# Optimization experiments

Hardware: AMD Instinct MI355X
Metric: run time of the kernel (lower is better)

Reference implementation:

```python
import jax, jax.numpy as jnp
import numpy as np

K = 16          # neighbors per point
POINTNUM = 2048 # opt.pointnum
B, N = 8, 2048


def _knn_concat(x, k):
    """x: [B,N,C] -> [B,N,k,2C] = concat(center, k-nearest neighbor feats)."""
    sq = jnp.sum(x * x, axis=-1)                                   # [B,N]
    d2 = sq[:, :, None] + sq[:, None, :] - 2.0 * jnp.einsum('bnc,bmc->bnm', x, x)
    _, idx = jax.lax.top_k(-d2, k)                                 # [B,N,k]
    nbr = jax.vmap(lambda xb, ib: xb[ib])(x, idx)                  # [B,N,k,C]
    ctr = jnp.broadcast_to(x[:, :, None, :], nbr.shape)
    return jnp.concatenate([ctr, nbr], axis=-1)


def _lin(x, w, b):
    return x @ w + b


lrelu = jax.nn.leaky_relu  # default negative_slope=0.01 matches nn.LeakyReLU()


def setup_inputs() -> dict:
    key = jax.random.key(0)
    ks = jax.random.split(key, 20)

    def w(k_, fi, fo):
        return jax.random.normal(k_, (fi, fo), jnp.float32) / np.sqrt(fi)

    inp = {
        'x': jax.random.normal(ks[0], (B, N, 3), jnp.float32),
        'h1w1': w(ks[1], 6, 16),   'h1b1': jnp.zeros((16,), jnp.float32),
        'h1w2': w(ks[2], 16, 64),  'h1b2': jnp.zeros((64,), jnp.float32),
        'h1w3': w(ks[3], 64, 32),  'h1b3': jnp.zeros((32,), jnp.float32),
        'h2w1': w(ks[4], 64, 256), 'h2b1': jnp.zeros((256,), jnp.float32),
        'h2w2': w(ks[5], 256, 128),'h2b2': jnp.zeros((128,), jnp.float32),
        'h3w1': w(ks[6], 256, 128),'h3b1': jnp.zeros((128,), jnp.float32),
        'fc1w': w(ks[7], 128, 128),'fc1b': jnp.zeros((128,), jnp.float32),
        'fc2w': w(ks[8], 128, 128),'fc2b': jnp.zeros((128,), jnp.float32),
        'fc3w': w(ks[9], 128, POINTNUM * 3), 'fc3b': jnp.zeros((POINTNUM * 3,), jnp.float32),
    }
    return inp


def reference(x, h1w1, h1b1, h1w2, h1b2, h1w3, h1b3,
              h2w1, h2b1, h2w2, h2b2, h3w1, h3b1,
              fc1w, fc1b, fc2w, fc2b, fc3w, fc3b):
    # block 1: knn-concat [B,N,K,6] -> MLP(6,16,64,32) -> sum over K
    x1 = _knn_concat(x, K)
    h = lrelu(_lin(x1, h1w1, h1b1))
    h = lrelu(_lin(h, h1w2, h1b2))
    h = lrelu(_lin(h, h1w3, h1b3))
    x2 = jnp.sum(h, axis=2)                    # [B,N,32]
    # block 2: [B,N,K,64] -> MLP(64,256,128) -> sum over K
    x2 = _knn_concat(x2, K)
    h = lrelu(_lin(x2, h2w1, h2b1))
    h = lrelu(_lin(h, h2w2, h2b2))
    x3 = jnp.sum(h, axis=2)                    # [B,N,128]
    # block 3: [B,N,K,256] -> MLP(256,128) -> sum over K
    x3 = _knn_concat(x3, K)
    h = lrelu(_lin(x3, h3w1, h3b1))
    x4 = jnp.sum(h, axis=2)                    # [B,N,128]
    # global max pool over points
    x5 = jnp.max(x4, axis=1)                   # [B,128]
    x6 = lrelu(_lin(x5, fc1w, fc1b))
    x7 = lrelu(_lin(x6, fc2w, fc2b))
    x8 = _lin(x7, fc3w, fc3b)                  # [B, POINTNUM*3]
    return x8.reshape(x8.shape[0], POINTNUM, 3)
```

## Files before the change

kernel.cpp:

```cpp
#include <hip/hip_runtime.h>

#define KNB 16
#define BSZ 8
#define NPT 2048

typedef __attribute__((ext_vector_type(8))) short bf16x8;
typedef __attribute__((ext_vector_type(4))) float f32x4;

__device__ __forceinline__ float lrelu(float x) { return x >= 0.f ? x : 0.01f * x; }

__device__ __forceinline__ unsigned short bf16rne(float f) {
    union { float f; unsigned int u; } v; v.f = f;
    return (unsigned short)((v.u + 0x7FFFu + ((v.u >> 16) & 1u)) >> 16);
}

__device__ __forceinline__ float packkey(float d, int idx) {
    union { float f; unsigned int u; } v; v.f = d;
    v.u = (v.u & 0xFFFFF800u) | (unsigned int)idx;
    return v.f;
}

__device__ __forceinline__ void ceA(float& a, float& b) {
    const float lo = fminf(a, b), hi = fmaxf(a, b);
    a = lo; b = hi;
}

__device__ __forceinline__ void bsort16(float* c) {
#pragma unroll
    for (int k = 2; k <= 16; k <<= 1) {
#pragma unroll
        for (int j = k >> 1; j > 0; j >>= 1) {
#pragma unroll
            for (int i = 0; i < 16; ++i) {
                const int l = i ^ j;
                if (l > i) {
                    if ((i & k) == 0) ceA(c[i], c[l]);
                    else              ceA(c[l], c[i]);
                }
            }
        }
    }
}

__device__ __forceinline__ void merge16(float* L, const float* C) {
#pragma unroll
    for (int i = 0; i < 16; ++i) L[i] = fminf(L[i], C[15 - i]);
#pragma unroll
    for (int j = 8; j > 0; j >>= 1) {
#pragma unroll
        for (int i = 0; i < 16; ++i) {
            const int l = i ^ j;
            if (l > i) ceA(L[i], L[l]);
        }
    }
}

__device__ __forceinline__ void st16(float* dst, const float* L) {
#pragma unroll
    for (int c = 0; c < 4; ++c)
        *(f32x4*)(dst + c * 4) = (f32x4){L[c * 4], L[c * 4 + 1], L[c * 4 + 2], L[c * 4 + 3]};
}

__device__ __forceinline__ void ld16(float* L, const float* src) {
#pragma unroll
    for (int c = 0; c < 4; ++c) {
        const f32x4 v = *(const f32x4*)(src + c * 4);
        L[c * 4] = v[0]; L[c * 4 + 1] = v[1]; L[c * 4 + 2] = v[2]; L[c * 4 + 3] = v[3];
    }
}

__device__ __forceinline__ void xwave_merge_out(float (*sS)[20], int w, int lane,
                                                float* L, float* outp) {
    st16(sS[w * 64 + lane], L);
    __syncthreads();
    if ((w & 1) == 0) {
        float C[16];
        ld16(C, sS[(w + 1) * 64 + lane]);
        merge16(L, C);
        if (w == 2) st16(sS[2 * 64 + lane], L);
    }
    __syncthreads();
    if (w == 0) {
        float C[16];
        ld16(C, sS[2 * 64 + lane]);
        merge16(L, C);
        st16(outp, L);
    }
}

__global__ void wprep_kernel(const float* __restrict__ w, unsigned short* __restrict__ wt,
                             int K, int N) {
    int i = blockIdx.x * 256 + threadIdx.x;
    if (i < K * N) { int k = i / N, n = i - k * N; wt[n * K + k] = bf16rne(w[i]); }
}

__global__ void wprep_b1_kernel(const float* __restrict__ w1, const float* __restrict__ w2,
                                const float* __restrict__ w3,
                                unsigned short* __restrict__ w1a, unsigned short* __restrict__ w2a,
                                unsigned short* __restrict__ w3a) {
    int i = blockIdx.x * 256 + threadIdx.x;
    if (i < 512) {
        int n = i >> 5, k = i & 31;
        w1a[i] = (k < 6) ? bf16rne(w1[k * 16 + n]) : (unsigned short)0;
    } else if (i < 2560) {
        int j = i - 512, n = j >> 5, k = j & 31;
        w2a[j] = (k < 16) ? bf16rne(w2[k * 64 + n]) : (unsigned short)0;
    } else if (i < 4608) {
        int j = i - 2560, n = j >> 6, k = j & 63;
        w3a[j] = bf16rne(w3[k * 32 + n]);
    }
}

template<int C>
__global__ void norms16_kernel(const unsigned short* __restrict__ feat, float* __restrict__ out) {
    int gid = blockIdx.x * blockDim.x + threadIdx.x;
    if (gid < BSZ * NPT) {
        const unsigned short* p = feat + (size_t)gid * C;
        float s = 0.f;
#pragma unroll
        for (int c8 = 0; c8 < C / 8; ++c8) {
            const bf16x8 v = *(const bf16x8*)(p + c8 * 8);
#pragma unroll
            for (int j = 0; j < 8; ++j) {
                union { unsigned int u; float f; } t;
                t.u = ((unsigned int)(unsigned short)v[j]) << 16;
                s = fmaf(t.f, t.f, s);
            }
        }
        out[gid] = s;
    }
}

template<int C>
__global__ void norms_kernel(const float* __restrict__ feat, float* __restrict__ out) {
    int gid = blockIdx.x * blockDim.x + threadIdx.x;
    if (gid < BSZ * NPT) {
        const float* p = feat + (size_t)gid * C;
        float s = 0.f;
#pragma unroll
        for (int c = 0; c < C; ++c) s = fmaf(p[c], p[c], s);
        out[gid] = s;
    }
}

template<int JS>
__launch_bounds__(256, 3)
__global__ void knn3_kernel(const float* __restrict__ feat,
                            const float* __restrict__ norms,
                            float* __restrict__ cand) {
    constexpr int JL = NPT / JS;
    constexpr int JP = JL / 4;
    const int b = blockIdx.z, js = blockIdx.y, i0 = blockIdx.x * 64;
    const int t = threadIdx.x, w = t >> 6, lane = t & 63;
    const float* fb = feat + (size_t)b * NPT * 3;
    const float* nb = norms + (size_t)b * NPT;

    __shared__ __align__(16) float sS[256][20];

    float q0, q1, q2;
    { const float* qp = fb + (size_t)(i0 + lane) * 3; q0 = qp[0]; q1 = qp[1]; q2 = qp[2]; }

    float L[16];
#pragma unroll
    for (int u = 0; u < 16; ++u) L[u] = 3e38f;

    const int jbeg = js * JL + w * JP;
#pragma unroll 1
    for (int j0 = jbeg; j0 < jbeg + JP; j0 += 16) {
        float C[16];
#pragma unroll
        for (int u = 0; u < 16; ++u) {
            const int j = j0 + u;
            const float* pp = fb + (size_t)j * 3;
            C[u] = packkey(fmaf(-2.f, fmaf(q0, pp[0], fmaf(q1, pp[1], q2 * pp[2])), nb[j]), j);
        }
        bsort16(C);
        merge16(L, C);
    }
    float* o = cand + (((size_t)b * NPT + i0 + lane) * JS + js) * 16;
    xwave_merge_out(sS, w, lane, L, o);
}

template<int C, int JS>
__launch_bounds__(256, 3)
__global__ void knn_mfma_kernel(const unsigned short* __restrict__ fb16,
                                const float* __restrict__ norms,
                                float* __restrict__ cand) {
    constexpr int JL = NPT / JS;
    constexpr int KS = C / 32;
    const int b    = blockIdx.z;
    const int js   = blockIdx.y;
    const int i0   = blockIdx.x * 64;
    const int t    = threadIdx.x;
    const int w    = t >> 6;
    const int lane = t & 63;
    const int l15  = lane & 15;
    const int quad = lane >> 4;
    const unsigned short* fbb = fb16 + (size_t)b * NPT * C;
    const float* nb = norms + (size_t)b * NPT;

    __shared__ __align__(16) float sS[256][20];

    bf16x8 afr[KS * 4];
#pragma unroll
    for (int ks = 0; ks < KS; ++ks)
#pragma unroll
        for (int mi = 0; mi < 4; ++mi)
            afr[ks * 4 + mi] = *(const bf16x8*)(fbb + (size_t)(i0 + mi * 16 + l15) * C + ks * 32 + quad * 8);

    float L[16];
#pragma unroll
    for (int u = 0; u < 16; ++u) L[u] = 3e38f;

    const int jbeg = js * JL;
#pragma unroll 1
    for (int j0 = jbeg; j0 < jbeg + JL; j0 += 64) {
        f32x4 acc[4];
#pragma unroll
        for (int mi = 0; mi < 4; ++mi) acc[mi] = (f32x4){0.f, 0.f, 0.f, 0.f};
        const unsigned short* prow = fbb + (size_t)(j0 + w * 16 + l15) * C + quad * 8;
#pragma unroll
        for (int ks = 0; ks < KS; ++ks) {
            const bf16x8 bfr = *(const bf16x8*)(prow + ks * 32);
#pragma unroll
            for (int mi = 0; mi < 4; ++mi)
                acc[mi] = __builtin_amdgcn_mfma_f32_16x16x32_bf16(afr[ks * 4 + mi], bfr, acc[mi], 0, 0, 0);
        }
        const float nv  = nb[j0 + w * 16 + l15];
        const int  cidx = j0 + w * 16 + l15;
#pragma unroll
        for (int mi = 0; mi < 4; ++mi)
#pragma unroll
            for (int r = 0; r < 4; ++r)
                sS[w * 64 + mi * 16 + quad * 4 + r][l15] = packkey(fmaf(-2.f, acc[mi][r], nv), cidx);
        float Cb[16];
        ld16(Cb, sS[w * 64 + lane]);
        bsort16(Cb);
        merge16(L, Cb);
    }

    float* o = cand + (((size_t)b * NPT + i0 + lane) * JS + js) * 16;
    xwave_merge_out(sS, w, lane, L, o);
}

template<int JS>
__launch_bounds__(256)
__global__ void knn_merge_kernel(const float* __restrict__ cand, int* __restrict__ knn_out) {
    const int q = blockIdx.x * 256 + threadIdx.x;
    const float* pd = cand + (size_t)q * JS * 16;
    float L[16];
    ld16(L, pd);
#pragma unroll
    for (int s = 1; s < JS; ++s) {
        float C[16];
        ld16(C, pd + s * 16);
        merge16(L, C);
    }
    int* o = knn_out + (size_t)q * KNB;
#pragma unroll
    for (int u = 0; u < 16; ++u) {
        union { float f; unsigned int v; } z; z.f = L[u];
        o[u] = (int)(z.v & 2047u);
    }
}

__launch_bounds__(256, 3)
__global__ void block1_mfma_kernel(const float* __restrict__ x, const int* __restrict__ knn,
                                   const unsigned short* __restrict__ w1a, const float* __restrict__ b1,
                                   const unsigned short* __restrict__ w2a, const float* __restrict__ b2,
                                   const unsigned short* __restrict__ w3a, const float* __restrict__ b3,
                                   unsigned short* __restrict__ x2b) {
    const int w = threadIdx.x >> 6, lane = threadIdx.x & 63;
    const int l15 = lane & 15, quad = lane >> 4;

    const bf16x8 W1 = *(const bf16x8*)(w1a + l15 * 32 + quad * 8);
    bf16x8 W2[4];
#pragma unroll
    for (int nt = 0; nt < 4; ++nt)
        W2[nt] = *(const bf16x8*)(w2a + (nt * 16 + l15) * 32 + quad * 8);
    bf16x8 W3[2][2];
#pragma unroll
    for (int tt = 0; tt < 2; ++tt)
#pragma unroll
        for (int ks = 0; ks < 2; ++ks)
            W3[tt][ks] = *(const bf16x8*)(w3a + (tt * 16 + l15) * 64 + ks * 32 + quad * 8);
    float b1v[4], b2v[4][4], b3v[2][4];
#pragma unroll
    for (int r = 0; r < 4; ++r) b1v[r] = b1[quad * 4 + r];
#pragma unroll
    for (int nt = 0; nt < 4; ++nt)
#pragma unroll
        for (int r = 0; r < 4; ++r) b2v[nt][r] = b2[nt * 16 + quad * 4 + r];
#pragma unroll
    for (int tt = 0; tt < 2; ++tt)
#pragma unroll
        for (int r = 0; r < 4; ++r) b3v[tt][r] = b3[tt * 16 + quad * 4 + r];

    const int src0 = ((2 * quad) & 3) * 16 + l15;
    const int src1 = ((2 * quad + 1) & 3) * 16 + l15;
    const int ntsel = quad >> 1;

    const int p0 = blockIdx.x * 16 + w * 4;
#pragma unroll 2
    for (int pi = 0; pi < 4; ++pi) {
        const int p = p0 + pi, b = p >> 11, n = p & (NPT - 1);
        int d0 = 0, d1 = 0, d2 = 0;
        if (quad == 0) {
            const float* xc = x + ((size_t)b * NPT + n) * 3;
            const int jn = knn[(size_t)p * KNB + l15];
            const float* xn = x + ((size_t)b * NPT + jn) * 3;
            const unsigned s0 = bf16rne(xc[0]), s1 = bf16rne(xc[1]), s2 = bf16rne(xc[2]);
            const unsigned s3 = bf16rne(xn[0]), s4 = bf16rne(xn[1]), s5 = bf16rne(xn[2]);
            d0 = (int)(s0 | (s1 << 16));
            d1 = (int)(s2 | (s3 << 16));
            d2 = (int)(s4 | (s5 << 16));
        }
        union { int i[4]; bf16x8 v; } B1;
        B1.i[0] = d0; B1.i[1] = d1; B1.i[2] = d2; B1.i[3] = 0;
        const f32x4 a1 = __builtin_amdgcn_mfma_f32_16x16x32_bf16(W1, B1.v, (f32x4){0.f, 0.f, 0.f, 0.f}, 0, 0, 0);

        int h10, h11;
        {
            const unsigned t0 = bf16rne(lrelu(a1[0] + b1v[0]));
            const unsigned t1 = bf16rne(lrelu(a1[1] + b1v[1]));
            const unsigned t2 = bf16rne(lrelu(a1[2] + b1v[2]));
            const unsigned t3 = bf16rne(lrelu(a1[3] + b1v[3]));
            h10 = (int)(t0 | (t1 << 16));
            h11 = (int)(t2 | (t3 << 16));
        }
        union { int i[4]; bf16x8 v; } B2;
        {
            const int e0 = __shfl(h10, src0), e1 = __shfl(h11, src0);
            const int e2 = __shfl(h10, src1), e3 = __shfl(h11, src1);
            const bool val = quad < 2;
            B2.i[0] = val ? e0 : 0; B2.i[1] = val ? e1 : 0;
            B2.i[2] = val ? e2 : 0; B2.i[3] = val ? e3 : 0;
        }
        f32x4 a2[4];
#pragma unroll
        for (int nt = 0; nt < 4; ++nt)
            a2[nt] = __builtin_amdgcn_mfma_f32_16x16x32_bf16(W2[nt], B2.v, (f32x4){0.f, 0.f, 0.f, 0.f}, 0, 0, 0);
        int dpk[4][2];
#pragma unroll
        for (int nt = 0; nt < 4; ++nt) {
            const unsigned t0 = bf16rne(lrelu(a2[nt][0] + b2v[nt][0]));
            const unsigned t1 = bf16rne(lrelu(a2[nt][1] + b2v[nt][1]));
            const unsigned t2 = bf16rne(lrelu(a2[nt][2] + b2v[nt][2]));
            const unsigned t3 = bf16rne(lrelu(a2[nt][3] + b2v[nt][3]));
            dpk[nt][0] = (int)(t0 | (t1 << 16));
            dpk[nt][1] = (int)(t2 | (t3 << 16));
        }
        f32x4 a3[2] = { (f32x4){0.f, 0.f, 0.f, 0.f}, (f32x4){0.f, 0.f, 0.f, 0.f} };
#pragma unroll
        for (int ks = 0; ks < 2; ++ks) {
            union { int i[4]; bf16x8 v; } B3;
            const int a0l = __shfl(dpk[2 * ks][0], src0), a0h = __shfl(dpk[2 * ks + 1][0], src0);
            const int a1l = __shfl(dpk[2 * ks][1], src0), a1h = __shfl(dpk[2 * ks + 1][1], src0);
            const int a2l = __shfl(dpk[2 * ks][0], src1), a2h = __shfl(dpk[2 * ks + 1][0], src1);
            const int a3l = __shfl(dpk[2 * ks][1], src1), a3h = __shfl(dpk[2 * ks + 1][1], src1);
            B3.i[0] = ntsel ? a0h : a0l;
            B3.i[1] = ntsel ? a1h : a1l;
            B3.i[2] = ntsel ? a2h : a2l;
            B3.i[3] = ntsel ? a3h : a3l;
#pragma unroll
            for (int tt = 0; tt < 2; ++tt)
                a3[tt] = __builtin_amdgcn_mfma_f32_16x16x32_bf16(W3[tt][ks], B3.v, a3[tt], 0, 0, 0);
        }
#pragma unroll
        for (int tt = 0; tt < 2; ++tt) {
#pragma unroll
            for (int r = 0; r < 4; ++r) {
                float s = lrelu(a3[tt][r] + b3v[tt][r]);
                s += __shfl_xor(s, 1);
                s += __shfl_xor(s, 2);
                s += __shfl_xor(s, 4);
                s += __shfl_xor(s, 8);
                if (l15 == 0)
                    x2b[(size_t)p * 32 + tt * 16 + quad * 4 + r] = bf16rne(s);
            }
        }
    }
}

__launch_bounds__(256, 2)
__global__ void block2_fused_kernel(const unsigned short* __restrict__ x2b,
                                    const int* __restrict__ knn,
                                    const unsigned short* __restrict__ w1t,
                                    const float* __restrict__ b1,
                                    const unsigned short* __restrict__ w2t,
                                    const float* __restrict__ b2,
                                    unsigned short* __restrict__ x3b) {
    const int w    = threadIdx.x >> 6;
    const int lane = threadIdx.x & 63;
    const int l15  = lane & 15, quad = lane >> 4;
    __shared__ __align__(16) unsigned short sH1[2][16][264];

    bf16x8 B1[4][2];
#pragma unroll
    for (int nt2 = 0; nt2 < 4; ++nt2)
#pragma unroll
        for (int ks = 0; ks < 2; ++ks)
            B1[nt2][ks] = *(const bf16x8*)(w1t + (size_t)(w * 64 + nt2 * 16 + l15) * 64 + ks * 32 + quad * 8);
    bf16x8 B2[2][8];
#pragma unroll
    for (int nt2 = 0; nt2 < 2; ++nt2)
#pragma unroll
        for (int ks = 0; ks < 8; ++ks)
            B2[nt2][ks] = *(const bf16x8*)(w2t + (size_t)(w * 32 + nt2 * 16 + l15) * 256 + ks * 32 + quad * 8);
    float b1v[4];
#pragma unroll
    for (int nt2 = 0; nt2 < 4; ++nt2) b1v[nt2] = b1[w * 64 + nt2 * 16 + l15];
    float b2v[2];
#pragma unroll
    for (int nt2 = 0; nt2 < 2; ++nt2) b2v[nt2] = b2[w * 32 + nt2 * 16 + l15];

    const int p0 = blockIdx.x * 8;
    const unsigned short* xb = x2b + (size_t)(p0 >> 11) * NPT * 32;

    int nbrv[8];
#pragma unroll
    for (int pi = 0; pi < 8; ++pi) nbrv[pi] = knn[(size_t)(p0 + pi) * KNB + l15];

    auto L1 = [&](const bf16x8& a0, const bf16x8& a1, int wbuf) {
#pragma unroll
        for (int nt2 = 0; nt2 < 4; ++nt2) {
            f32x4 acc = (f32x4){0.f, 0.f, 0.f, 0.f};
            acc = __builtin_amdgcn_mfma_f32_16x16x32_bf16(a0, B1[nt2][0], acc, 0, 0, 0);
            acc = __builtin_amdgcn_mfma_f32_16x16x32_bf16(a1, B1[nt2][1], acc, 0, 0, 0);
#pragma unroll
            for (int r = 0; r < 4; ++r)
                sH1[wbuf][quad * 4 + r][w * 64 + nt2 * 16 + l15] = bf16rne(lrelu(acc[r] + b1v[nt2]));
        }
    };
    auto L2 = [&](int p, int buf) {
        bf16x8 af[8];
#pragma unroll
        for (int ks = 0; ks < 8; ++ks)
            af[ks] = *(const bf16x8*)&sH1[buf][l15][ks * 32 + quad * 8];
#pragma unroll
        for (int nt2 = 0; nt2 < 2; ++nt2) {
            f32x4 acc = (f32x4){0.f, 0.f, 0.f, 0.f};
#pragma unroll
            for (int ks = 0; ks < 8; ++ks)
                acc = __builtin_amdgcn_mfma_f32_16x16x32_bf16(af[ks], B2[nt2][ks], acc, 0, 0, 0);
            float s = 0.f;
#pragma unroll
            for (int r = 0; r < 4; ++r) s += lrelu(acc[r] + b2v[nt2]);
            s += __shfl_xor(s, 16);
            s += __shfl_xor(s, 32);
            if (quad == 0) x3b[(size_t)p * 128 + w * 32 + nt2 * 16 + l15] = bf16rne(s);
        }
    };

    bf16x8 a0A = *(const bf16x8*)(x2b + (size_t)p0 * 32 + quad * 8);
    bf16x8 a1A = *(const bf16x8*)(xb + (size_t)nbrv[0] * 32 + quad * 8);
    bf16x8 a0B = *(const bf16x8*)(x2b + (size_t)(p0 + 1) * 32 + quad * 8);
    bf16x8 a1B = *(const bf16x8*)(xb + (size_t)nbrv[1] * 32 + quad * 8);
    L1(a0A, a1A, 0);

#pragma unroll
    for (int pj = 0; pj < 4; ++pj) {
        __syncthreads();
        L2(p0 + 2 * pj, 0);
        if (pj < 3) {
            a0A = *(const bf16x8*)(x2b + (size_t)(p0 + 2 * pj + 2) * 32 + quad * 8);
            a1A = *(const bf16x8*)(xb + (size_t)nbrv[2 * pj + 2] * 32 + quad * 8);
        }
        L1(a0B, a1B, 1);
        __syncthreads();
        L2(p0 + 2 * pj + 1, 1);
        if (pj < 3) {
            a0B = *(const bf16x8*)(x2b + (size_t)(p0 + 2 * pj + 3) * 32 + quad * 8);
            a1B = *(const bf16x8*)(xb + (size_t)nbrv[2 * pj + 3] * 32 + quad * 8);
            L1(a0A, a1A, 0);
        }
    }
}

__launch_bounds__(256, 3)
__global__ void block3_fused_kernel(const unsigned short* __restrict__ x3b,
                                    const int* __restrict__ knn,
                                    const unsigned short* __restrict__ w3t,
                                    const float* __restrict__ bias,
                                    float* __restrict__ x4) {
    const int w    = threadIdx.x >> 6;
    const int lane = threadIdx.x & 63;
    const int l15  = lane & 15, quad = lane >> 4;

    bf16x8 B3[2][8];
#pragma unroll
    for (int nt2 = 0; nt2 < 2; ++nt2)
#pragma unroll
        for (int ks = 0; ks < 8; ++ks)
            B3[nt2][ks] = *(const bf16x8*)(w3t + (size_t)(w * 32 + nt2 * 16 + l15) * 256 + ks * 32 + quad * 8);
    float bv[2];
#pragma unroll
    for (int nt2 = 0; nt2 < 2; ++nt2) bv[nt2] = bias[w * 32 + nt2 * 16 + l15];

    const int p0 = blockIdx.x * 8;
    const unsigned short* xb = x3b + (size_t)(p0 >> 11) * NPT * 128;

    int nbrv[8];
#pragma unroll
    for (int pi = 0; pi < 8; ++pi) nbrv[pi] = knn[(size_t)(p0 + pi) * KNB + l15];

    auto LDAF = [&](bf16x8* af, int pi, int nbr) {
        const unsigned short* ctr = x3b + (size_t)(p0 + pi) * 128 + quad * 8;
        const unsigned short* nbp = xb + (size_t)nbr * 128 + quad * 8;
#pragma unroll
        for (int ks = 0; ks < 4; ++ks) af[ks] = *(const bf16x8*)(ctr + ks * 32);
#pragma unroll
        for (int ks = 0; ks < 4; ++ks) af[4 + ks] = *(const bf16x8*)(nbp + ks * 32);
    };
    auto CMP = [&](int p, const bf16x8* af) {
#pragma unroll
        for (int nt2 = 0; nt2 < 2; ++nt2) {
            f32x4 acc = (f32x4){0.f, 0.f, 0.f, 0.f};
#pragma unroll
            for (int ks = 0; ks < 8; ++ks)
                acc = __builtin_amdgcn_mfma_f32_16x16x32_bf16(af[ks], B3[nt2][ks], acc, 0, 0, 0);
            float s = 0.f;
#pragma unroll
            for (int r = 0; r < 4; ++r) s += lrelu(acc[r] + bv[nt2]);
            s += __shfl_xor(s, 16);
            s += __shfl_xor(s, 32);
            if (quad == 0) x4[(size_t)p * 128 + w * 32 + nt2 * 16 + l15] = s;
        }
    };

    bf16x8 afA[8], afB[8];
    LDAF(afA, 0, nbrv[0]);
#pragma unroll
    for (int pj = 0; pj < 4; ++pj) {
        LDAF(afB, 2 * pj + 1, nbrv[2 * pj + 1]);
        CMP(p0 + 2 * pj, afA);
        if (pj < 3) LDAF(afA, 2 * pj + 2, nbrv[2 * pj + 2]);
        CMP(p0 + 2 * pj + 1, afB);
    }
}

__launch_bounds__(128)
__global__ void maxpool_partial_kernel(const float* __restrict__ x4,
                                       float* __restrict__ part) {
    const int chunk = blockIdx.x, b = blockIdx.y, t = threadIdx.x;
    const float* xb = x4 + ((size_t)b * NPT + (size_t)chunk * 128) * 128;
    float m = -1e30f;
#pragma unroll 8
    for (int n = 0; n < 128; ++n) m = fmaxf(m, xb[(size_t)n * 128 + t]);
    part[((size_t)b * 16 + chunk) * 128 + t] = m;
}

__launch_bounds__(128)
__global__ void head2_kernel(const float* __restrict__ part,
                             const float* __restrict__ fc1w, const float* __restrict__ fc1b,
                             const float* __restrict__ fc2w, const float* __restrict__ fc2b,
                             const float* __restrict__ fc3w, const float* __restrict__ fc3b,
                             float* __restrict__ out) {
    const int g = blockIdx.x, b = blockIdx.y, t = threadIdx.x;
    __shared__ float s5[128], s6[128], s7[128];
    float m = -1e30f;
#pragma unroll
    for (int c = 0; c < 16; ++c)
        m = fmaxf(m, part[((size_t)b * 16 + c) * 128 + t]);
    s5[t] = m;
    __syncthreads();
    float a = fc1b[t];
#pragma unroll 4
    for (int i = 0; i < 128; ++i) a = fmaf(s5[i], fc1w[i * 128 + t], a);
    s6[t] = lrelu(a);
    __syncthreads();
    a = fc2b[t];
#pragma unroll 4
    for (int i = 0; i < 128; ++i) a = fmaf(s6[i], fc2w[i * 128 + t], a);
    s7[t] = lrelu(a);
    __syncthreads();
    const int o = g * 128 + t;
    float acc = fc3b[o];
#pragma unroll 4
    for (int i = 0; i < 128; ++i) acc = fmaf(s7[i], fc3w[(size_t)i * 6144 + o], acc);
    out[(size_t)b * 6144 + o] = acc;
}

extern "C" void kernel_launch(void* const* d_in, const int* in_sizes, int n_in,
                              void* d_out, int out_size, void* d_ws, size_t ws_size,
                              hipStream_t stream) {
    const float* x    = (const float*)d_in[0];
    const float* h1w1 = (const float*)d_in[1];
    const float* h1b1 = (const float*)d_in[2];
    const float* h1w2 = (const float*)d_in[3];
    const float* h1b2 = (const float*)d_in[4];
    const float* h1w3 = (const float*)d_in[5];
    const float* h1b3 = (const float*)d_in[6];
    const float* h2w1 = (const float*)d_in[7];
    const float* h2b1 = (const float*)d_in[8];
    const float* h2w2 = (const float*)d_in[9];
    const float* h2b2 = (const float*)d_in[10];
    const float* h3w1 = (const float*)d_in[11];
    const float* h3b1 = (const float*)d_in[12];
    const float* fc1w = (const float*)d_in[13];
    const float* fc1b = (const float*)d_in[14];
    const float* fc2w = (const float*)d_in[15];
    const float* fc2b = (const float*)d_in[16];
    const float* fc3w = (const float*)d_in[17];
    const float* fc3b = (const float*)d_in[18];

    float* ws = (float*)d_ws;
    unsigned short* x2b16 = (unsigned short*)ws;
    unsigned short* x3b16 = (unsigned short*)(ws + 262144);
    float* x4   = ws + 1310720;
    int*   idx  = (int*)(ws + 3407872);
    float* nrm  = ws + 3670016;
    float* part = ws + 3686400;
    unsigned short* w1t = (unsigned short*)(ws + 3702784);
    unsigned short* w2t = (unsigned short*)(ws + 3710976);
    unsigned short* w3t = (unsigned short*)(ws + 3727360);
    unsigned short* w1a = (unsigned short*)(ws + 3743744);
    unsigned short* w2a = (unsigned short*)(ws + 3744000);
    unsigned short* w3a = (unsigned short*)(ws + 3745024);
    float* cd   = ws + 3746048;
    float* out  = (float*)d_out;

    const dim3 kg(32, 4, 8);

    wprep_kernel<<<64, 256, 0, stream>>>(h2w1, w1t, 64, 256);
    wprep_kernel<<<128, 256, 0, stream>>>(h2w2, w2t, 256, 128);
    wprep_kernel<<<128, 256, 0, stream>>>(h3w1, w3t, 256, 128);
    wprep_b1_kernel<<<18, 256, 0, stream>>>(h1w1, h1w2, h1w3, w1a, w2a, w3a);

    norms_kernel<3><<<64, 256, 0, stream>>>(x, nrm);
    knn3_kernel<4><<<kg, 256, 0, stream>>>(x, nrm, cd);
    knn_merge_kernel<4><<<64, 256, 0, stream>>>(cd, idx);
    block1_mfma_kernel<<<1024, 256, 0, stream>>>(x, idx, w1a, h1b1, w2a, h1b2, w3a, h1b3, x2b16);

    norms16_kernel<32><<<64, 256, 0, stream>>>(x2b16, nrm);
    knn_mfma_kernel<32, 4><<<kg, 256, 0, stream>>>(x2b16, nrm, cd);
    knn_merge_kernel<4><<<64, 256, 0, stream>>>(cd, idx);
    block2_fused_kernel<<<BSZ * NPT / 8, 256, 0, stream>>>(x2b16, idx, w1t, h2b1, w2t, h2b2, x3b16);

    norms16_kernel<128><<<64, 256, 0, stream>>>(x3b16, nrm);
    knn_mfma_kernel<128, 4><<<kg, 256, 0, stream>>>(x3b16, nrm, cd);
    knn_merge_kernel<4><<<64, 256, 0, stream>>>(cd, idx);
    block3_fused_kernel<<<BSZ * NPT / 8, 256, 0, stream>>>(x3b16, idx, w3t, h3b1, x4);

    maxpool_partial_kernel<<<dim3(16, 8), 128, 0, stream>>>(x4, part);
    head2_kernel<<<dim3(48, 8), 128, 0, stream>>>(part, fc1w, fc1b, fc2w, fc2b,
                                                  fc3w, fc3b, out);
}
```

Baseline: 376.1 us.

## Batch block2 layer-1 for all eight points before a single barrier

Block2 kernel now loads all eight points' gathered inputs up front, runs layer 1 for all of them into an eight-slot shared buffer, and does one barrier before running layer 2 for all points. This replaces the two-buffer ping-pong with seven barriers, aiming to cut synchronisation stalls and expose more independent gathers at once. The shared buffer grows from about 17 KB to about 68 KB per block and register pressure rises from the 16 held input vectors, which may reduce occupancy below the declared two blocks per CU.

```diff
diff --git a/kernel.cpp b/kernel.cpp
--- a/kernel.cpp
+++ b/kernel.cpp
@@ -393,7 +393,7 @@
     const int w    = threadIdx.x >> 6;
     const int lane = threadIdx.x & 63;
     const int l15  = lane & 15, quad = lane >> 4;
-    __shared__ __align__(16) unsigned short sH1[2][16][264];
+    __shared__ __align__(16) unsigned short sH1[8][16][264];
 
     bf16x8 B1[4][2];
 #pragma unroll
@@ -421,22 +421,34 @@
 #pragma unroll
     for (int pi = 0; pi < 8; ++pi) nbrv[pi] = knn[(size_t)(p0 + pi) * KNB + l15];
 
-    auto L1 = [&](const bf16x8& a0, const bf16x8& a1, int wbuf) {
+    bf16x8 a0[8], a1[8];
+#pragma unroll
+    for (int pi = 0; pi < 8; ++pi) {
+        a0[pi] = *(const bf16x8*)(x2b + (size_t)(p0 + pi) * 32 + quad * 8);
+        a1[pi] = *(const bf16x8*)(xb + (size_t)nbrv[pi] * 32 + quad * 8);
+    }
+
+#pragma unroll
+    for (int pi = 0; pi < 8; ++pi) {
 #pragma unroll
         for (int nt2 = 0; nt2 < 4; ++nt2) {
             f32x4 acc = (f32x4){0.f, 0.f, 0.f, 0.f};
-            acc = __builtin_amdgcn_mfma_f32_16x16x32_bf16(a0, B1[nt2][0], acc, 0, 0, 0);
-            acc = __builtin_amdgcn_mfma_f32_16x16x32_bf16(a1, B1[nt2][1], acc, 0, 0, 0);
+            acc = __builtin_amdgcn_mfma_f32_16x16x32_bf16(a0[pi], B1[nt2][0], acc, 0, 0, 0);
+            acc = __builtin_amdgcn_mfma_f32_16x16x32_bf16(a1[pi], B1[nt2][1], acc, 0, 0, 0);
 #pragma unroll
             for (int r = 0; r < 4; ++r)
-                sH1[wbuf][quad * 4 + r][w * 64 + nt2 * 16 + l15] = bf16rne(lrelu(acc[r] + b1v[nt2]));
-        }
-    };
-    auto L2 = [&](int p, int buf) {
+                sH1[pi][quad * 4 + r][w * 64 + nt2 * 16 + l15] = bf16rne(lrelu(acc[r] + b1v[nt2]));
+        }
+    }
+
+    __syncthreads();
+
+#pragma unroll
+    for (int pi = 0; pi < 8; ++pi) {
         bf16x8 af[8];
 #pragma unroll
         for (int ks = 0; ks < 8; ++ks)
-            af[ks] = *(const bf16x8*)&sH1[buf][l15][ks * 32 + quad * 8];
+            af[ks] = *(const bf16x8*)&sH1[pi][l15][ks * 32 + quad * 8];
 #pragma unroll
         for (int nt2 = 0; nt2 < 2; ++nt2) {
             f32x4 acc = (f32x4){0.f, 0.f, 0.f, 0.f};
@@ -448,31 +460,7 @@
             for (int r = 0; r < 4; ++r) s += lrelu(acc[r] + b2v[nt2]);
             s += __shfl_xor(s, 16);
             s += __shfl_xor(s, 32);
-            if (quad == 0) x3b[(size_t)p * 128 + w * 32 + nt2 * 16 + l15] = bf16rne(s);
-        }
-    };
-
-    bf16x8 a0A = *(const bf16x8*)(x2b + (size_t)p0 * 32 + quad * 8);
-    bf16x8 a1A = *(const bf16x8*)(xb + (size_t)nbrv[0] * 32 + quad * 8);
-    bf16x8 a0B = *(const bf16x8*)(x2b + (size_t)(p0 + 1) * 32 + quad * 8);
-    bf16x8 a1B = *(const bf16x8*)(xb + (size_t)nbrv[1] * 32 + quad * 8);
-    L1(a0A, a1A, 0);
-
-#pragma unroll
-    for (int pj = 0; pj < 4; ++pj) {
-        __syncthreads();
-        L2(p0 + 2 * pj, 0);
-        if (pj < 3) {
-            a0A = *(const bf16x8*)(x2b + (size_t)(p0 + 2 * pj + 2) * 32 + quad * 8);
-            a1A = *(const bf16x8*)(xb + (size_t)nbrv[2 * pj + 2] * 32 + quad * 8);
-        }
-        L1(a0B, a1B, 1);
-        __syncthreads();
-        L2(p0 + 2 * pj + 1, 1);
-        if (pj < 3) {
-            a0B = *(const bf16x8*)(x2b + (size_t)(p0 + 2 * pj + 3) * 32 + quad * 8);
-            a1B = *(const bf16x8*)(xb + (size_t)nbrv[2 * pj + 3] * 32 + quad * 8);
-            L1(a0A, a1A, 0);
+            if (quad == 0) x3b[(size_t)(p0 + pi) * 128 + w * 32 + nt2 * 16 + l15] = bf16rne(s);
         }
     }
 }
```

Result: no change. 374.2 us (-0.5%).
